# Kernel optimization log

Measured on AMD Instinct MI355X. Metric: run time of the kernel, lower is better.

The kernel has to match this reference:

```python
import jax, jax.numpy as jnp
import numpy as np

NEG_INF = -jnp.inf


def conv2d(x, w, b, stride, pad):
    # x: [B,C,H,W], w: [O,I,kh,kw]
    y = jax.lax.conv_general_dilated(
        x, w, window_strides=(stride, stride),
        padding=[(pad, pad), (pad, pad)],
        dimension_numbers=('NCHW', 'OIHW', 'NCHW'))
    return y + b[None, :, None, None]


def maxpool3s2(x):
    return jax.lax.reduce_window(x, -jnp.inf, jax.lax.max,
                                 (1, 1, 3, 3), (1, 1, 2, 2), 'VALID')


def setup_inputs() -> dict:
    key = jax.random.key(0)
    ks = jax.random.split(key, 20)
    s = 0.02
    B, C, H, W = 64, 3, 224, 224
    D, HID, OUT, E = 9216, 288, 1000, 8   # feature_dim, hidden_dim, output_dim, n_experts
    GH = 72                               # gate hidden = hidden_dim // 4
    inp = {
        'x':   jax.random.normal(ks[0], (B, C, H, W), jnp.float32),
        'c1w': s * jax.random.normal(ks[1], (64, 3, 11, 11), jnp.float32),
        'c1b': jnp.zeros((64,), jnp.float32),
        'c2w': s * jax.random.normal(ks[2], (192, 64, 5, 5), jnp.float32),
        'c2b': jnp.zeros((192,), jnp.float32),
        'c3w': s * jax.random.normal(ks[3], (384, 192, 3, 3), jnp.float32),
        'c3b': jnp.zeros((384,), jnp.float32),
        'c4w': s * jax.random.normal(ks[4], (256, 384, 3, 3), jnp.float32),
        'c4b': jnp.zeros((256,), jnp.float32),
        'c5w': s * jax.random.normal(ks[5], (256, 256, 3, 3), jnp.float32),
        'c5b': jnp.zeros((256,), jnp.float32),
        'gw1': s * jax.random.normal(ks[6], (D, GH), jnp.float32),
        'gb1': jnp.zeros((GH,), jnp.float32),
        'gw2': s * jax.random.normal(ks[7], (GH, E), jnp.float32),
        'gb2': jnp.zeros((E,), jnp.float32),
        'ew1': s * jax.random.normal(ks[8], (E, D, HID), jnp.float32),
        'eb1': jnp.zeros((E, HID), jnp.float32),
        'ew2': s * jax.random.normal(ks[9], (E, HID, HID // 2), jnp.float32),
        'eb2': jnp.zeros((E, HID // 2), jnp.float32),
        'ew3': s * jax.random.normal(ks[10], (E, HID // 2, OUT), jnp.float32),
        'eb3': jnp.zeros((E, OUT), jnp.float32),
    }
    return inp


def reference(x, c1w, c1b, c2w, c2b, c3w, c3b, c4w, c4b, c5w, c5b,
              gw1, gb1, gw2, gb2, ew1, eb1, ew2, eb2, ew3, eb3):
    # ---- AlexNet-style feature extractor (224 branch) ----
    h = jax.nn.relu(conv2d(x, c1w, c1b, 4, 2))   # [B,64,55,55]
    h = maxpool3s2(h)                             # [B,64,27,27]
    h = jax.nn.relu(conv2d(h, c2w, c2b, 1, 2))   # [B,192,27,27]
    h = maxpool3s2(h)                             # [B,192,13,13]
    h = jax.nn.relu(conv2d(h, c3w, c3b, 1, 1))   # [B,384,13,13]
    h = jax.nn.relu(conv2d(h, c4w, c4b, 1, 1))   # [B,256,13,13]
    h = jax.nn.relu(conv2d(h, c5w, c5b, 1, 1))   # [B,256,13,13]
    h = maxpool3s2(h)                             # [B,256,6,6]
    # AdaptiveAvgPool2d((6,6)) on a 6x6 input is the identity.
    feat = h.reshape(h.shape[0], -1)              # [B,9216]

    # ---- Gate: top-2 routing (eval mode: no noise, no dropout) ----
    g = jax.nn.relu(feat @ gw1 + gb1)             # [B,72]
    logits = g @ gw2 + gb2                        # [B,8]
    topv, topi = jax.lax.top_k(logits, 2)         # [B,2]
    topw = jax.nn.softmax(topv, axis=-1)          # softmax over top-2 only
    B = logits.shape[0]
    gates = jnp.zeros_like(logits).at[jnp.arange(B)[:, None], topi].set(topw)  # [B,8]

    # ---- Dense per-expert 3-layer MLP over full batch (as in source) ----
    h1 = jax.nn.relu(jnp.einsum('bd,edh->ebh', feat, ew1) + eb1[:, None, :])   # [E,B,288]
    h2 = jax.nn.relu(jnp.einsum('ebh,ehk->ebk', h1, ew2) + eb2[:, None, :])    # [E,B,144]
    eo = jnp.einsum('ebk,eko->ebo', h2, ew3) + eb3[:, None, :]                 # [E,B,1000]
    # Weighted combine; gates are zero for non-top-2 experts, matching the
    # masked accumulation loop in the torch forward.
    out = jnp.einsum('ebo,be->bo', eo, gates)     # [B,1000]
    return out
```

## Files before the change

kernel.cpp:

```cpp
#include <hip/hip_runtime.h>
#include <math.h>

#define TPB 256

typedef short s16x8 __attribute__((ext_vector_type(8)));
typedef short s16x4 __attribute__((ext_vector_type(4)));
typedef float f32x4 __attribute__((ext_vector_type(4)));

__device__ inline void bsplit(float x, short& h, short& l){
  union { float f; unsigned u; } a, hf, rf;
  a.f = x;
  unsigned hu = (a.u + 0x7FFFu + ((a.u >> 16) & 1u)) >> 16;
  h = (short)hu;
  hf.u = hu << 16;
  rf.f = x - hf.f;
  l = (short)((rf.u + 0x7FFFu + ((rf.u >> 16) & 1u)) >> 16);
}
__device__ inline float b2f(short s){
  union { unsigned u; float f; } x;
  x.u = ((unsigned)(unsigned short)s) << 16;
  return x.f;
}

__global__ __launch_bounds__(TPB) void wsplit_k(
    const float* __restrict__ w, short* __restrict__ wh, short* __restrict__ wl,
    int C, int O, int ntap, int total)
{
  int idx = blockIdx.x*TPB + threadIdx.x;
  if (idx >= total) return;
  int c   = idx % C;
  int t2  = idx / C;
  int oc  = t2 % O;
  int tap = t2 / O;
  float x = w[((size_t)oc*C + c)*ntap + tap];
  short h, l; bsplit(x, h, l);
  int tile = oc >> 4, ln = oc & 15;
  int S    = ntap*(C >> 5);
  int sl   = tap*(C >> 5) + (c >> 5);
  int lg   = (c >> 3) & 3, j = c & 7;
  size_t dst = (((size_t)tile*S + sl)*64 + lg*16 + ln)*8 + j;
  wh[dst] = h; wl[dst] = l;
}

__global__ __launch_bounds__(TPB) void wsplit1_k(
    const float* __restrict__ w, short* __restrict__ wh, short* __restrict__ wl)
{
  int idx = blockIdx.x*TPB + threadIdx.x;
  if (idx >= 64*576) return;
  int k  = idx % 576;
  int oc = idx / 576;
  int g  = k >> 4, kw = k & 15;
  int c  = g / 12, kh = g % 12;
  float x = 0.f;
  if (kh < 11 && kw < 11)
    x = w[((size_t)oc*3 + c)*121 + kh*11 + kw];
  short h, l; bsplit(x, h, l);
  int m = oc >> 4, ln = oc & 15;
  int s = k >> 5, r = k & 31;
  int lg = r >> 3, j = r & 7;
  size_t dst = (((size_t)m*18 + s)*64 + lg*16 + ln)*8 + j;
  wh[dst] = h; wl[dst] = l;
}

__global__ __launch_bounds__(TPB) void wtrans_k(
    const float* __restrict__ w, float* __restrict__ wT, int K, int O)
{
  int idx = blockIdx.x*TPB + threadIdx.x;
  if (idx >= K*O) return;
  int oc = idx % O;
  int k  = idx / O;
  wT[idx] = w[(size_t)oc*K + k];
}

#define C1W 240
#define CV1_PL 33
__global__ __launch_bounds__(256, 2) void conv1m_k(
    const float* __restrict__ in, const short* __restrict__ whi,
    const short* __restrict__ wlo, const float* __restrict__ bias,
    short* __restrict__ yh, short* __restrict__ yl)
{
  __shared__ __align__(16) short lds[2][CV1_PL*C1W + 84];
  const int tid = threadIdx.x;
  const int oh = blockIdx.x % 55;
  const int b  = blockIdx.x / 55;
  const int nt = tid >> 6;
  const int ln = tid & 15;
  const int lg = (tid & 63) >> 4;
  const int lane = tid & 63;
  const int ow = nt*16 + ln;

  const float* ip = in + (size_t)b*3*224*224;
  for (int i = tid; i < CV1_PL*59; i += 256){
    int plane = i / 59;
    int p     = i % 59;
    int c = plane / 11, kh = plane % 11;
    int ih = oh*4 - 2 + kh;
    int col0 = p*4;
    const float* rowp = (ih >= 0 && ih < 224) ? ip + (size_t)c*50176 + (size_t)ih*224 : nullptr;
    short h[4], l[4];
    #pragma unroll
    for (int j=0;j<4;++j){
      int iw = col0 + j - 2;
      float v = (rowp && iw >= 0 && iw < 224) ? rowp[iw] : 0.f;
      bsplit(v, h[j], l[j]);
    }
    s16x4 hv = {h[0],h[1],h[2],h[3]}, lv = {l[0],l[1],l[2],l[3]};
    *reinterpret_cast<s16x4*>(&lds[0][plane*C1W + col0]) = hv;
    *reinterpret_cast<s16x4*>(&lds[1][plane*C1W + col0]) = lv;
  }
  __syncthreads();

  f32x4 acc[4];
  #pragma unroll
  for (int m=0;m<4;++m){
    const float4 bv = *reinterpret_cast<const float4*>(bias + m*16 + lg*4);
    acc[m] = (f32x4){bv.x, bv.y, bv.z, bv.w};
  }

  s16x8 ah[4], al[4], ahn[4], aln[4];
  #pragma unroll
  for (int m=0;m<4;++m){
    size_t ao = (((size_t)m*18 + 0)*64 + lane)*8;
    ah[m] = *reinterpret_cast<const s16x8*>(whi + ao);
    al[m] = *reinterpret_cast<const s16x8*>(wlo + ao);
  }

  #pragma unroll 1
  for (int s=0; s<18; ++s){
    if (s < 17){
      #pragma unroll
      for (int m=0;m<4;++m){
        size_t ao = (((size_t)m*18 + s + 1)*64 + lane)*8;
        ahn[m] = *reinterpret_cast<const s16x8*>(whi + ao);
        aln[m] = *reinterpret_cast<const s16x8*>(wlo + ao);
      }
    }
    int g  = 2*s + (lg >> 1);
    int c  = g / 12, kh = g % 12;
    int plane = c*11 + (kh < 11 ? kh : 10);
    int base  = plane*C1W + ow*4 + (lg & 1)*8;
    s16x4 h0 = *reinterpret_cast<const s16x4*>(&lds[0][base]);
    s16x4 h1 = *reinterpret_cast<const s16x4*>(&lds[0][base+4]);
    s16x4 l0 = *reinterpret_cast<const s16x4*>(&lds[1][base]);
    s16x4 l1 = *reinterpret_cast<const s16x4*>(&lds[1][base+4]);
    s16x8 bh = __builtin_shufflevector(h0, h1, 0,1,2,3,4,5,6,7);
    s16x8 bl = __builtin_shufflevector(l0, l1, 0,1,2,3,4,5,6,7);
    #pragma unroll
    for (int m=0;m<4;++m){
      acc[m] = __builtin_amdgcn_mfma_f32_16x16x32_bf16(al[m], bh, acc[m], 0,0,0);
      acc[m] = __builtin_amdgcn_mfma_f32_16x16x32_bf16(ah[m], bl, acc[m], 0,0,0);
      acc[m] = __builtin_amdgcn_mfma_f32_16x16x32_bf16(ah[m], bh, acc[m], 0,0,0);
    }
    #pragma unroll
    for (int m=0;m<4;++m){ ah[m] = ahn[m]; al[m] = aln[m]; }
  }

  if (ow < 55){
    size_t base = ((size_t)b*3025 + (size_t)oh*55 + ow)*64;
    #pragma unroll
    for (int m=0;m<4;++m){
      short h[4], l[4];
      #pragma unroll
      for (int r=0;r<4;++r) bsplit(fmaxf(acc[m][r], 0.f), h[r], l[r]);
      s16x4 hv = {h[0],h[1],h[2],h[3]}, lv = {l[0],l[1],l[2],l[3]};
      *reinterpret_cast<s16x4*>(yh + base + m*16 + lg*4) = hv;
      *reinterpret_cast<s16x4*>(yl + base + m*16 + lg*4) = lv;
    }
  }
}

__global__ __launch_bounds__(TPB) void pool1_k(
    const short* __restrict__ xh, const short* __restrict__ xl,
    short* __restrict__ yh, short* __restrict__ yl)
{
  int i = blockIdx.x*TPB + threadIdx.x;
  if (i >= 64*729*64) return;
  int c = i & 63;
  int t = i >> 6;
  int sp = t % 729;
  int b = t / 729;
  int r = sp/27, cc = sp%27;
  const short* ph = xh + (size_t)b*3025*64 + c;
  const short* pl = xl + (size_t)b*3025*64 + c;
  float m = -INFINITY;
  #pragma unroll
  for (int di=0;di<3;++di)
    #pragma unroll
    for (int dj=0;dj<3;++dj){
      size_t s = (size_t)((2*r+di)*55 + 2*cc+dj)*64;
      m = fmaxf(m, b2f(ph[s]) + b2f(pl[s]));
    }
  short h, l; bsplit(m, h, l);
  yh[i] = h; yl[i] = l;
}

__global__ __launch_bounds__(256, 3) void conv2m_k(
    const short* __restrict__ xh, const short* __restrict__ xl,
    const short* __restrict__ whi, const short* __restrict__ wlo,
    const float* __restrict__ bias, short* __restrict__ yh, short* __restrict__ yl)
{
  __shared__ __align__(16) short lds[2][217*40];
  const int tid = threadIdx.x;
  const int rg  = blockIdx.x;
  const int b   = blockIdx.y;
  const int wid = tid >> 6;
  const int ln  = tid & 15;
  const int lg  = (tid & 63) >> 4;
  const int lane = tid & 63;
  const int oc0 = wid*48;
  const int r0  = rg*3;

  int sb[6], nn[6];
  #pragma unroll
  for (int t=0;t<6;++t){
    int n = t*16 + ln;
    nn[t] = n;
    int ohl = n / 27, ow = n % 27;
    sb[t] = (n < 81) ? (ohl*31 + ow) : 0;
  }

  f32x4 acc[3][6];
  #pragma unroll
  for (int m=0;m<3;++m){
    const float4 bv = *reinterpret_cast<const float4*>(bias + oc0 + m*16 + lg*4);
    #pragma unroll
    for (int t=0;t<6;++t) acc[m][t] = (f32x4){bv.x, bv.y, bv.z, bv.w};
  }

  #pragma unroll 1
  for (int c0=0; c0<64; c0+=32){
    __syncthreads();
    for (int i = tid; i < 217*4; i += 256){
      int sp = i >> 2, v = i & 3;
      int pr = sp/31, pc = sp%31;
      int ih = r0 - 2 + pr, iw = pc - 2;
      s16x8 hv = {0,0,0,0,0,0,0,0}, lv = {0,0,0,0,0,0,0,0};
      if (ih >= 0 && ih < 27 && iw >= 0 && iw < 27){
        size_t o = ((size_t)b*729 + ih*27 + iw)*64 + c0 + v*8;
        hv = *reinterpret_cast<const s16x8*>(xh + o);
        lv = *reinterpret_cast<const s16x8*>(xl + o);
      }
      *reinterpret_cast<s16x8*>(&lds[0][sp*40 + v*8]) = hv;
      *reinterpret_cast<s16x8*>(&lds[1][sp*40 + v*8]) = lv;
    }
    __syncthreads();

    const size_t tstr = 50*512;
    const size_t abase = ((size_t)(wid*3)*50 + (c0 >> 5))*512 + (size_t)lane*8;
    s16x8 ah0 = *reinterpret_cast<const s16x8*>(whi + abase);
    s16x8 ah1 = *reinterpret_cast<const s16x8*>(whi + abase + tstr);
    s16x8 ah2 = *reinterpret_cast<const s16x8*>(whi + abase + 2*tstr);
    s16x8 al0 = *reinterpret_cast<const s16x8*>(wlo + abase);
    s16x8 al1 = *reinterpret_cast<const s16x8*>(wlo + abase + tstr);
    s16x8 al2 = *reinterpret_cast<const s16x8*>(wlo + abase + 2*tstr);

    #pragma unroll 1
    for (int tap=0; tap<25; ++tap){
      s16x8 nh0=ah0, nh1=ah1, nh2=ah2, nl0=al0, nl1=al1, nl2=al2;
      if (tap < 24){
        size_t ao = abase + (size_t)(tap+1)*2*512;
        nh0 = *reinterpret_cast<const s16x8*>(whi + ao);
        nh1 = *reinterpret_cast<const s16x8*>(whi + ao + tstr);
        nh2 = *reinterpret_cast<const s16x8*>(whi + ao + 2*tstr);
        nl0 = *reinterpret_cast<const s16x8*>(wlo + ao);
        nl1 = *reinterpret_cast<const s16x8*>(wlo + ao + tstr);
        nl2 = *reinterpret_cast<const s16x8*>(wlo + ao + 2*tstr);
      }
      const int toff = (tap/5)*31 + (tap%5);
      #pragma unroll
      for (int t=0;t<6;++t){
        int off = (sb[t] + toff)*40 + lg*8;
        s16x8 bh = *reinterpret_cast<const s16x8*>(&lds[0][off]);
        s16x8 bl = *reinterpret_cast<const s16x8*>(&lds[1][off]);
        acc[0][t] = __builtin_amdgcn_mfma_f32_16x16x32_bf16(al0, bh, acc[0][t], 0,0,0);
        acc[0][t] = __builtin_amdgcn_mfma_f32_16x16x32_bf16(ah0, bl, acc[0][t], 0,0,0);
        acc[0][t] = __builtin_amdgcn_mfma_f32_16x16x32_bf16(ah0, bh, acc[0][t], 0,0,0);
        acc[1][t] = __builtin_amdgcn_mfma_f32_16x16x32_bf16(al1, bh, acc[1][t], 0,0,0);
        acc[1][t] = __builtin_amdgcn_mfma_f32_16x16x32_bf16(ah1, bl, acc[1][t], 0,0,0);
        acc[1][t] = __builtin_amdgcn_mfma_f32_16x16x32_bf16(ah1, bh, acc[1][t], 0,0,0);
        acc[2][t] = __builtin_amdgcn_mfma_f32_16x16x32_bf16(al2, bh, acc[2][t], 0,0,0);
        acc[2][t] = __builtin_amdgcn_mfma_f32_16x16x32_bf16(ah2, bl, acc[2][t], 0,0,0);
        acc[2][t] = __builtin_amdgcn_mfma_f32_16x16x32_bf16(ah2, bh, acc[2][t], 0,0,0);
      }
      ah0=nh0; ah1=nh1; ah2=nh2; al0=nl0; al1=nl1; al2=nl2;
    }
  }

  #pragma unroll
  for (int m=0;m<3;++m)
    #pragma unroll
    for (int t=0;t<6;++t){
      if (nn[t] < 81){
        int gsp = r0*27 + nn[t];
        size_t base = ((size_t)b*729 + gsp)*192 + oc0 + m*16 + lg*4;
        short h[4], l[4];
        #pragma unroll
        for (int r=0;r<4;++r) bsplit(fmaxf(acc[m][t][r], 0.f), h[r], l[r]);
        s16x4 hv = {h[0],h[1],h[2],h[3]}, lv = {l[0],l[1],l[2],l[3]};
        *reinterpret_cast<s16x4*>(yh + base) = hv;
        *reinterpret_cast<s16x4*>(yl + base) = lv;
      }
    }
}

__global__ __launch_bounds__(TPB) void pool2_k(
    const short* __restrict__ xh, const short* __restrict__ xl,
    short* __restrict__ yh, short* __restrict__ yl)
{
  int i = blockIdx.x*TPB + threadIdx.x;
  if (i >= 64*169*192) return;
  int c = i % 192;
  int t = i / 192;
  int sp = t % 169;
  int b = t / 169;
  int r = sp/13, cc = sp%13;
  const short* ph = xh + (size_t)b*729*192 + c;
  const short* pl = xl + (size_t)b*729*192 + c;
  float m = -INFINITY;
  #pragma unroll
  for (int di=0;di<3;++di)
    #pragma unroll
    for (int dj=0;dj<3;++dj){
      size_t s = (size_t)((2*r+di)*27 + 2*cc+dj)*192;
      m = fmaxf(m, b2f(ph[s]) + b2f(pl[s]));
    }
  short h, l; bsplit(m, h, l);
  yh[i] = h; yl[i] = l;
}

template<int C,int O>
__global__ __launch_bounds__(256, 3) void conv3m_k(
    const short* __restrict__ xh, const short* __restrict__ xl,
    const short* __restrict__ whi, const short* __restrict__ wlo,
    const float* __restrict__ bias, short* __restrict__ yh, short* __restrict__ yl)
{
  __shared__ __align__(16) short lds[2][225*40];
  const int tid = threadIdx.x;
  const int b   = blockIdx.y;
  const int wid = tid >> 6;
  const int ln  = tid & 15;
  const int lg  = (tid & 63) >> 4;
  const int lane = tid & 63;
  const int tileIdx = blockIdx.x*2 + (wid & 1);
  const int oc0 = tileIdx*16;
  const int ng  = wid >> 1;
  const int tbase  = ng ? 6 : 0;
  const int ntiles = ng ? 5 : 6;
  const int S3 = 9*(C/32);

  int sb[6], nn[6];
  #pragma unroll
  for (int t=0;t<6;++t){
    int n = (tbase + t)*16 + ln;
    nn[t] = n;
    int oh = n / 13, ow = n % 13;
    sb[t] = (n < 169) ? (oh*15 + ow) : 0;
  }

  f32x4 acc[6];
  const float4 bv = *reinterpret_cast<const float4*>(bias + oc0 + lg*4);
  #pragma unroll
  for (int t=0;t<6;++t) acc[t] = (f32x4){bv.x, bv.y, bv.z, bv.w};

  #pragma unroll 1
  for (int c0=0; c0<C; c0+=32){
    __syncthreads();
    for (int i = tid; i < 225*4; i += 256){
      int sp = i >> 2, v = i & 3;
      int r = sp/15, cc = sp%15;
      s16x8 hv = {0,0,0,0,0,0,0,0}, lv = {0,0,0,0,0,0,0,0};
      if (r >= 1 && r <= 13 && cc >= 1 && cc <= 13){
        size_t o = ((size_t)b*169 + (r-1)*13 + (cc-1))*C + c0 + v*8;
        hv = *reinterpret_cast<const s16x8*>(xh + o);
        lv = *reinterpret_cast<const s16x8*>(xl + o);
      }
      *reinterpret_cast<s16x8*>(&lds[0][sp*40 + v*8]) = hv;
      *reinterpret_cast<s16x8*>(&lds[1][sp*40 + v*8]) = lv;
    }
    __syncthreads();

    const size_t tb = (size_t)tileIdx*S3 + (c0 >> 5);
    s16x8 ah = *reinterpret_cast<const s16x8*>(whi + (tb*64 + lane)*8);
    s16x8 al = *reinterpret_cast<const s16x8*>(wlo + (tb*64 + lane)*8);
    #pragma unroll 1
    for (int tap=0; tap<9; ++tap){
      s16x8 ahn = ah, aln = al;
      if (tap < 8){
        size_t ao = ((tb + (size_t)(tap+1)*(C/32))*64 + lane)*8;
        ahn = *reinterpret_cast<const s16x8*>(whi + ao);
        aln = *reinterpret_cast<const s16x8*>(wlo + ao);
      }
      const int toff = (tap/3)*15 + (tap%3);
      #pragma unroll
      for (int t=0;t<6;++t){
        if (t < ntiles){
          int off = (sb[t] + toff)*40 + lg*8;
          s16x8 bh = *reinterpret_cast<const s16x8*>(&lds[0][off]);
          s16x8 bl = *reinterpret_cast<const s16x8*>(&lds[1][off]);
          acc[t] = __builtin_amdgcn_mfma_f32_16x16x32_bf16(al, bh, acc[t], 0,0,0);
          acc[t] = __builtin_amdgcn_mfma_f32_16x16x32_bf16(ah, bl, acc[t], 0,0,0);
          acc[t] = __builtin_amdgcn_mfma_f32_16x16x32_bf16(ah, bh, acc[t], 0,0,0);
        }
      }
      ah = ahn; al = aln;
    }
  }

  #pragma unroll
  for (int t=0;t<6;++t){
    if (t < ntiles && nn[t] < 169){
      size_t base = ((size_t)b*169 + nn[t])*O + oc0 + lg*4;
      short h[4], l[4];
      #pragma unroll
      for (int r=0;r<4;++r) bsplit(fmaxf(acc[t][r], 0.f), h[r], l[r]);
      s16x4 hv = {h[0],h[1],h[2],h[3]}, lv = {l[0],l[1],l[2],l[3]};
      *reinterpret_cast<s16x4*>(yh + base) = hv;
      *reinterpret_cast<s16x4*>(yl + base) = lv;
    }
  }
}

__global__ __launch_bounds__(TPB) void pool3_k(
    const short* __restrict__ xh, const short* __restrict__ xl,
    float* __restrict__ feat)
{
  int i = blockIdx.x*TPB + threadIdx.x;
  if (i >= 64*9216) return;
  int d = i % 9216;
  int b = i / 9216;
  int c = d / 36;
  int sp = d % 36;
  int r = sp/6, cc = sp%6;
  const short* ph = xh + (size_t)b*169*256 + c;
  const short* pl = xl + (size_t)b*169*256 + c;
  float m = -INFINITY;
  #pragma unroll
  for (int di=0;di<3;++di)
    #pragma unroll
    for (int dj=0;dj<3;++dj){
      size_t s = (size_t)((2*r+di)*13 + 2*cc+dj)*256;
      m = fmaxf(m, b2f(ph[s]) + b2f(pl[s]));
    }
  feat[i] = m;
}

__global__ __launch_bounds__(256) void gate1_k(
    const float* __restrict__ feat, const float* __restrict__ gw1T,
    const float* __restrict__ gb1, float* __restrict__ g)
{
  const int b    = blockIdx.x;
  const int h    = blockIdx.y*4 + (threadIdx.x >> 6);
  const int lane = threadIdx.x & 63;
  const float* f = feat + (size_t)b*9216;
  const float* w = gw1T + (size_t)h*9216;
  float s = 0.f;
  #pragma unroll
  for (int it=0; it<36; ++it){
    int d = it*256 + lane*4;
    float4 fv = *reinterpret_cast<const float4*>(f + d);
    float4 wv = *reinterpret_cast<const float4*>(w + d);
    s = fmaf(fv.x, wv.x, s);
    s = fmaf(fv.y, wv.y, s);
    s = fmaf(fv.z, wv.z, s);
    s = fmaf(fv.w, wv.w, s);
  }
  #pragma unroll
  for (int off=32; off; off>>=1) s += __shfl_down(s, off, 64);
  if (lane == 0) g[(size_t)b*72 + h] = fmaxf(s + gb1[h], 0.f);
}

__global__ __launch_bounds__(128) void gate2_k(
    const float* __restrict__ g, const float* __restrict__ gw2,
    const float* __restrict__ gb2, float* __restrict__ gates)
{
  const int b = blockIdx.x;
  const int tid = threadIdx.x;
  __shared__ float gs[72];
  __shared__ float logits[8];
  if (tid < 72) gs[tid] = g[(size_t)b*72 + tid];
  __syncthreads();
  if (tid < 8) {
    float acc = gb2[tid];
    for (int j=0;j<72;++j)
      acc = fmaf(gs[j], gw2[(size_t)j*8 + tid], acc);
    logits[tid] = acc;
  }
  __syncthreads();
  if (tid == 0) {
    int i1 = 0; float v1 = logits[0];
    for (int e=1;e<8;++e) if (logits[e] > v1) { v1 = logits[e]; i1 = e; }
    int i2 = -1; float v2 = -INFINITY;
    for (int e=0;e<8;++e) { if (e==i1) continue; if (logits[e] > v2) { v2 = logits[e]; i2 = e; } }
    float z  = expf(v2 - v1);
    float w1 = 1.f / (1.f + z);
    float w2 = z   / (1.f + z);
    float* gr = gates + (size_t)b*8;
    for (int e=0;e<8;++e) gr[e] = 0.f;
    gr[i1] = w1;
    gr[i2] = w2;
  }
}

__global__ __launch_bounds__(256, 2) void eh1_part_k(
    const float* __restrict__ feat, const float* __restrict__ ew1,
    float* __restrict__ part)
{
  const int e  = blockIdx.x;
  const int ks = blockIdx.y;
  const int nb = blockIdx.z;
  const int h0 = nb*144;
  __shared__ __align__(16) float fs[64*33];
  __shared__ __align__(16) float wsh[32*144];
  const int tid = threadIdx.x;
  const int tx = tid & 15;
  const int ty = tid >> 4;
  float acc[4][9];
  #pragma unroll
  for (int i=0;i<4;++i)
    #pragma unroll
    for (int j=0;j<9;++j) acc[i][j]=0.f;
  const float* wbase = ew1 + (size_t)e*9216*288 + h0;
  for (int d0 = ks*192; d0 < ks*192+192; d0 += 32){
    __syncthreads();
    for (int l = tid; l < 512; l += 256){
      int r = l >> 3, c = l & 7;
      float4 v = *reinterpret_cast<const float4*>(feat + (size_t)r*9216 + d0 + c*4);
      float* dst = &fs[r*33 + c*4];
      dst[0]=v.x; dst[1]=v.y; dst[2]=v.z; dst[3]=v.w;
    }
    for (int l = tid; l < 1152; l += 256){
      int r = l / 36, c = l % 36;
      *reinterpret_cast<float4*>(&wsh[r*144 + c*4]) =
        *reinterpret_cast<const float4*>(wbase + (size_t)(d0 + r)*288 + c*4);
    }
    __syncthreads();
    #pragma unroll
    for (int k=0;k<32;++k){
      float fv[4], wv[9];
      #pragma unroll
      for (int i=0;i<4;++i) fv[i] = fs[(ty*4+i)*33 + k];
      #pragma unroll
      for (int j=0;j<9;++j) wv[j] = wsh[k*144 + tx*9 + j];
      #pragma unroll
      for (int i=0;i<4;++i)
        #pragma unroll
        for (int j=0;j<9;++j)
          acc[i][j] = fmaf(fv[i], wv[j], acc[i][j]);
    }
  }
  float* pp = part + (size_t)(ks*8 + e)*64*288;
  #pragma unroll
  for (int i=0;i<4;++i)
    #pragma unroll
    for (int j=0;j<9;++j)
      pp[(ty*4+i)*288 + h0 + tx*9 + j] = acc[i][j];
}

__global__ __launch_bounds__(TPB) void eh1_reduce_k(
    const float* __restrict__ part, const float* __restrict__ eb1,
    float* __restrict__ h1)
{
  int idx = blockIdx.x*TPB + threadIdx.x;
  if (idx >= 8*64*288) return;
  int h = idx % 288;
  int e = idx / (64*288);
  float a = eb1[(size_t)e*288 + h];
  #pragma unroll
  for (int s=0;s<48;++s)
    a += part[(size_t)s*147456 + idx];
  h1[idx] = fmaxf(a, 0.f);
}

__global__ __launch_bounds__(TPB) void expert_h2_k(
    const float* __restrict__ h1, const float* __restrict__ ew2,
    const float* __restrict__ eb2, const float* __restrict__ gates,
    float* __restrict__ h2)
{
  int idx = blockIdx.x*TPB + threadIdx.x;
  if (idx >= 8*64*144) return;
  int k = idx % 144;
  int t = idx / 144;
  int b = t % 64;
  int e = t / 64;
  if (gates[(size_t)b*8 + e] == 0.f) return;
  float acc = eb2[(size_t)e*144 + k];
  const float* h = h1 + ((size_t)e*64 + b)*288;
  const float* w = ew2 + (size_t)e*288*144 + k;
  for (int d=0; d<288; ++d)
    acc = fmaf(h[d], w[(size_t)d*144], acc);
  h2[idx] = fmaxf(acc, 0.f);
}

__global__ __launch_bounds__(TPB) void expert_out_k(
    const float* __restrict__ h2, const float* __restrict__ ew3,
    const float* __restrict__ eb3, const float* __restrict__ gates,
    float* __restrict__ out)
{
  int idx = blockIdx.x*TPB + threadIdx.x;
  if (idx >= 64*1000) return;
  int o = idx % 1000;
  int b = idx / 1000;
  float acc = 0.f;
  const float* gr = gates + (size_t)b*8;
  for (int e=0;e<8;++e){
    float ge = gr[e];
    if (ge == 0.f) continue;
    float a = eb3[(size_t)e*1000 + o];
    const float* h = h2 + ((size_t)e*64 + b)*144;
    const float* w = ew3 + (size_t)e*144*1000 + o;
    for (int k=0;k<144;++k)
      a = fmaf(h[k], w[(size_t)k*1000], a);
    acc = fmaf(ge, a, acc);
  }
  out[idx] = acc;
}

static inline int nblk(long long n){ return (int)((n + TPB - 1) / TPB); }

extern "C" void kernel_launch(void* const* d_in, const int* in_sizes, int n_in,
                              void* d_out, int out_size, void* d_ws, size_t ws_size,
                              hipStream_t stream)
{
  const float* x   = (const float*)d_in[0];
  const float* c1w = (const float*)d_in[1];  const float* c1b = (const float*)d_in[2];
  const float* c2w = (const float*)d_in[3];  const float* c2b = (const float*)d_in[4];
  const float* c3w = (const float*)d_in[5];  const float* c3b = (const float*)d_in[6];
  const float* c4w = (const float*)d_in[7];  const float* c4b = (const float*)d_in[8];
  const float* c5w = (const float*)d_in[9];  const float* c5b = (const float*)d_in[10];
  const float* gw1 = (const float*)d_in[11]; const float* gb1 = (const float*)d_in[12];
  const float* gw2 = (const float*)d_in[13]; const float* gb2 = (const float*)d_in[14];
  const float* ew1 = (const float*)d_in[15]; const float* eb1 = (const float*)d_in[16];
  const float* ew2 = (const float*)d_in[17]; const float* eb2 = (const float*)d_in[18];
  const float* ew3 = (const float*)d_in[19]; const float* eb3 = (const float*)d_in[20];
  float* out = (float*)d_out;

  float* W = (float*)d_ws;
  short* X1H = (short*)W;
  short* X1L = X1H + 12390400;
  short* X3H = (short*)W;
  short* X3L = X3H + 8957952;
  short* X5H = (short*)W;
  short* X5L = X5H + 4153344;
  short* X7H = (short*)W;
  short* X7L = X7H + 2768896;
  float* feat  = W + 5000000;
  float* part  = W + 6000000;
  short* WH2 = (short*)(W +  9000000);
  short* WL2 = WH2 + 307200;
  short* WH3 = (short*)(W +  9320000);
  short* WL3 = WH3 + 663552;
  short* WH4 = (short*)(W + 10000000);
  short* WL4 = WH4 + 884736;
  short* WH5 = (short*)(W + 10900000);
  short* WL5 = WH5 + 589824;
  float* GT1 = W + 11500000;
  short* X2H = (short*)(W + 12390400);
  short* X2L = X2H + 2985984;
  short* X4H = (short*)(W + 12390400);
  short* X4L = X4H + 2076672;
  short* X6H = (short*)(W + 12390400);
  short* X6L = X6H + 2768896;
  float* gates = W + 14000000;
  float* h1    = gates + 512;
  float* h2    = h1 + 147456;
  float* gbuf  = h2 + 73728;
  short* WH1 = (short*)(W + 15400000);
  short* WL1 = WH1 + 36864;
  (void)ws_size; (void)in_sizes; (void)n_in; (void)out_size;

  wsplit1_k<<<nblk(64LL*576), TPB, 0, stream>>>(c1w, WH1, WL1);
  conv1m_k<<<55*64, 256, 0, stream>>>(x, WH1, WL1, c1b, X1H, X1L);
  pool1_k<<<nblk(64LL*729*64), TPB, 0, stream>>>(X1H, X1L, X2H, X2L);
  wsplit_k<<<nblk(25LL*192*64),  TPB, 0, stream>>>(c2w, WH2, WL2,  64, 192, 25, 25*192*64);
  wsplit_k<<<nblk(9LL*384*192),  TPB, 0, stream>>>(c3w, WH3, WL3, 192, 384,  9, 9*384*192);
  wsplit_k<<<nblk(9LL*256*384),  TPB, 0, stream>>>(c4w, WH4, WL4, 384, 256,  9, 9*256*384);
  wsplit_k<<<nblk(9LL*256*256),  TPB, 0, stream>>>(c5w, WH5, WL5, 256, 256,  9, 9*256*256);
  wtrans_k<<<nblk(72LL*9216),    TPB, 0, stream>>>(gw1, GT1, 72, 9216);

  conv2m_k<<<dim3(9,64), 256, 0, stream>>>(X2H, X2L, WH2, WL2, c2b, X3H, X3L);
  pool2_k<<<nblk(64LL*169*192), TPB, 0, stream>>>(X3H, X3L, X4H, X4L);
  conv3m_k<192,384><<<dim3(12,64), 256, 0, stream>>>(X4H, X4L, WH3, WL3, c3b, X5H, X5L);
  conv3m_k<384,256><<<dim3(8,64),  256, 0, stream>>>(X5H, X5L, WH4, WL4, c4b, X6H, X6L);
  conv3m_k<256,256><<<dim3(8,64),  256, 0, stream>>>(X6H, X6L, WH5, WL5, c5b, X7H, X7L);
  pool3_k<<<nblk(64LL*9216), TPB, 0, stream>>>(X7H, X7L, feat);

  gate1_k<<<dim3(64,18), 256, 0, stream>>>(feat, GT1, gb1, gbuf);
  gate2_k<<<64, 128, 0, stream>>>(gbuf, gw2, gb2, gates);

  eh1_part_k<<<dim3(8,48,2), 256, 0, stream>>>(feat, ew1, part);
  eh1_reduce_k<<<nblk(8LL*64*288), TPB, 0, stream>>>(part, eb1, h1);
  expert_h2_k<<<nblk(8LL*64*144), TPB, 0, stream>>>(h1, ew2, eb2, gates, h2);
  expert_out_k<<<nblk(64LL*1000), TPB, 0, stream>>>(h2, ew3, eb3, gates, out);
}
```

Baseline: 585.1 us.

## Move expert layer-1 GEMM to split-bf16 MFMA and raise conv occupancy bounds

Replaces the FP32 SIMT expert first-layer GEMM (64x9216 by 8x9216x288) with an MFMA kernel that uses three-term bf16 hi/lo splitting. Features are pre-split into an MFMA-friendly layout by a new kernel, and weights are split on the fly into LDS. The split-K factor drops from 48 to 16, and the reduce kernel is adapted to the new partial layout. Separately, launch_bounds min-blocks on the conv kernels is raised to 4, which may force register spills.

```diff
diff --git a/kernel.cpp b/kernel.cpp
--- a/kernel.cpp
+++ b/kernel.cpp
@@ -74,7 +74,7 @@
 
 #define C1W 240
 #define CV1_PL 33
-__global__ __launch_bounds__(256, 2) void conv1m_k(
+__global__ __launch_bounds__(256, 4) void conv1m_k(
     const float* __restrict__ in, const short* __restrict__ whi,
     const short* __restrict__ wlo, const float* __restrict__ bias,
     short* __restrict__ yh, short* __restrict__ yl)
@@ -194,7 +194,7 @@
   yh[i] = h; yl[i] = l;
 }
 
-__global__ __launch_bounds__(256, 3) void conv2m_k(
+__global__ __launch_bounds__(256, 4) void conv2m_k(
     const short* __restrict__ xh, const short* __restrict__ xl,
     const short* __restrict__ whi, const short* __restrict__ wlo,
     const float* __restrict__ bias, short* __restrict__ yh, short* __restrict__ yl)
@@ -329,7 +329,7 @@
 }
 
 template<int C,int O>
-__global__ __launch_bounds__(256, 3) void conv3m_k(
+__global__ __launch_bounds__(256, 4) void conv3m_k(
     const short* __restrict__ xh, const short* __restrict__ xl,
     const short* __restrict__ whi, const short* __restrict__ wlo,
     const float* __restrict__ bias, short* __restrict__ yh, short* __restrict__ yl)
@@ -444,6 +444,21 @@
   feat[i] = m;
 }
 
+__global__ __launch_bounds__(TPB) void featsplit_k(
+    const float* __restrict__ feat, short* __restrict__ fbh, short* __restrict__ fbl)
+{
+  int idx = blockIdx.x*TPB + threadIdx.x;
+  if (idx >= 589824) return;
+  int j = idx & 7;
+  int lane = (idx >> 3) & 63;
+  int nt = (idx >> 9) & 3;
+  int s = idx >> 11;
+  int b = nt*16 + (lane & 15);
+  int d = s*32 + (lane >> 4)*8 + j;
+  short h, l; bsplit(feat[(size_t)b*9216 + d], h, l);
+  fbh[idx] = h; fbl[idx] = l;
+}
+
 __global__ __launch_bounds__(256) void gate1_k(
     const float* __restrict__ feat, const float* __restrict__ gw1T,
     const float* __restrict__ gb1, float* __restrict__ g)
@@ -501,59 +516,70 @@
   }
 }
 
-__global__ __launch_bounds__(256, 2) void eh1_part_k(
-    const float* __restrict__ feat, const float* __restrict__ ew1,
-    float* __restrict__ part)
-{
-  const int e  = blockIdx.x;
-  const int ks = blockIdx.y;
-  const int nb = blockIdx.z;
-  const int h0 = nb*144;
-  __shared__ __align__(16) float fs[64*33];
-  __shared__ __align__(16) float wsh[32*144];
+__global__ __launch_bounds__(256, 4) void eh1m_k(
+    const float* __restrict__ ew1, const short* __restrict__ fbh,
+    const short* __restrict__ fbl, float* __restrict__ part)
+{
+  __shared__ __align__(16) short wh_l[32*88];
+  __shared__ __align__(16) short wl_l[32*88];
+  const int m2 = blockIdx.x;
+  const int e  = blockIdx.y;
+  const int ks = blockIdx.z;
   const int tid = threadIdx.x;
-  const int tx = tid & 15;
-  const int ty = tid >> 4;
-  float acc[4][9];
-  #pragma unroll
-  for (int i=0;i<4;++i)
-    #pragma unroll
-    for (int j=0;j<9;++j) acc[i][j]=0.f;
-  const float* wbase = ew1 + (size_t)e*9216*288 + h0;
-  for (int d0 = ks*192; d0 < ks*192+192; d0 += 32){
+  const int nt = tid >> 6;
+  const int ln = tid & 15;
+  const int lg = (tid & 63) >> 4;
+  const int lane = tid & 63;
+
+  f32x4 acc[2] = {(f32x4){0.f,0.f,0.f,0.f},(f32x4){0.f,0.f,0.f,0.f}};
+
+  const float* wsrc = ew1 + (size_t)e*9216*288 + (size_t)m2*32;
+  const int d0 = ks*576;
+
+  #pragma unroll 1
+  for (int st=0; st<9; ++st){
     __syncthreads();
-    for (int l = tid; l < 512; l += 256){
-      int r = l >> 3, c = l & 7;
-      float4 v = *reinterpret_cast<const float4*>(feat + (size_t)r*9216 + d0 + c*4);
-      float* dst = &fs[r*33 + c*4];
-      dst[0]=v.x; dst[1]=v.y; dst[2]=v.z; dst[3]=v.w;
-    }
-    for (int l = tid; l < 1152; l += 256){
-      int r = l / 36, c = l % 36;
-      *reinterpret_cast<float4*>(&wsh[r*144 + c*4]) =
-        *reinterpret_cast<const float4*>(wbase + (size_t)(d0 + r)*288 + c*4);
+    {
+      int drow = tid >> 2;
+      int h0 = (tid & 3)*8;
+      const float* src = wsrc + (size_t)(d0 + st*64 + drow)*288 + h0;
+      float4 v0 = *reinterpret_cast<const float4*>(src);
+      float4 v1 = *reinterpret_cast<const float4*>(src+4);
+      float vv[8] = {v0.x,v0.y,v0.z,v0.w,v1.x,v1.y,v1.z,v1.w};
+      #pragma unroll
+      for (int k=0;k<8;++k){
+        short h, l; bsplit(vv[k], h, l);
+        wh_l[(h0+k)*88 + drow] = h;
+        wl_l[(h0+k)*88 + drow] = l;
+      }
     }
     __syncthreads();
-    #pragma unroll
-    for (int k=0;k<32;++k){
-      float fv[4], wv[9];
+    int sg = (d0 + st*64) >> 5;
+    #pragma unroll
+    for (int sl=0; sl<2; ++sl){
+      size_t bo = ((size_t)(sg+sl)*4 + nt)*512 + (size_t)lane*8;
+      s16x8 bh = *reinterpret_cast<const s16x8*>(fbh + bo);
+      s16x8 bl = *reinterpret_cast<const s16x8*>(fbl + bo);
       #pragma unroll
-      for (int i=0;i<4;++i) fv[i] = fs[(ty*4+i)*33 + k];
-      #pragma unroll
-      for (int j=0;j<9;++j) wv[j] = wsh[k*144 + tx*9 + j];
-      #pragma unroll
-      for (int i=0;i<4;++i)
-        #pragma unroll
-        for (int j=0;j<9;++j)
-          acc[i][j] = fmaf(fv[i], wv[j], acc[i][j]);
-    }
-  }
-  float* pp = part + (size_t)(ks*8 + e)*64*288;
-  #pragma unroll
-  for (int i=0;i<4;++i)
-    #pragma unroll
-    for (int j=0;j<9;++j)
-      pp[(ty*4+i)*288 + h0 + tx*9 + j] = acc[i][j];
+      for (int m=0;m<2;++m){
+        int ao = (m*16 + ln)*88 + sl*32 + lg*8;
+        s16x8 ah = *reinterpret_cast<const s16x8*>(&wh_l[ao]);
+        s16x8 al = *reinterpret_cast<const s16x8*>(&wl_l[ao]);
+        acc[m] = __builtin_amdgcn_mfma_f32_16x16x32_bf16(al, bh, acc[m], 0,0,0);
+        acc[m] = __builtin_amdgcn_mfma_f32_16x16x32_bf16(ah, bl, acc[m], 0,0,0);
+        acc[m] = __builtin_amdgcn_mfma_f32_16x16x32_bf16(ah, bh, acc[m], 0,0,0);
+      }
+    }
+  }
+  #pragma unroll
+  for (int m=0;m<2;++m){
+    int h = m2*32 + m*16 + lg*4;
+    int b = nt*16 + ln;
+    float* pp = part + ((size_t)(ks*8+e)*288 + h)*64 + b;
+    #pragma unroll
+    for (int r=0;r<4;++r)
+      pp[(size_t)r*64] = acc[m][r];
+  }
 }
 
 __global__ __launch_bounds__(TPB) void eh1_reduce_k(
@@ -561,14 +587,15 @@
     float* __restrict__ h1)
 {
   int idx = blockIdx.x*TPB + threadIdx.x;
-  if (idx >= 8*64*288) return;
-  int h = idx % 288;
+  if (idx >= 8*288*64) return;
+  int b = idx & 63;
+  int h = (idx >> 6) % 288;
   int e = idx / (64*288);
   float a = eb1[(size_t)e*288 + h];
   #pragma unroll
-  for (int s=0;s<48;++s)
-    a += part[(size_t)s*147456 + idx];
-  h1[idx] = fmaxf(a, 0.f);
+  for (int s=0;s<16;++s)
+    a += part[((size_t)(s*8+e)*288 + h)*64 + b];
+  h1[((size_t)e*64 + b)*288 + h] = fmaxf(a, 0.f);
 }
 
 __global__ __launch_bounds__(TPB) void expert_h2_k(
@@ -644,7 +671,9 @@
   short* X7H = (short*)W;
   short* X7L = X7H + 2768896;
   float* feat  = W + 5000000;
-  float* part  = W + 6000000;
+  short* FBH   = (short*)(W + 5600000);
+  short* FBL   = (short*)(W + 5900000);
+  float* part  = W + 6300000;
   short* WH2 = (short*)(W +  9000000);
   short* WL2 = WH2 + 307200;
   short* WH3 = (short*)(W +  9320000);
@@ -687,8 +716,9 @@
   gate1_k<<<dim3(64,18), 256, 0, stream>>>(feat, GT1, gb1, gbuf);
   gate2_k<<<64, 128, 0, stream>>>(gbuf, gw2, gb2, gates);
 
-  eh1_part_k<<<dim3(8,48,2), 256, 0, stream>>>(feat, ew1, part);
-  eh1_reduce_k<<<nblk(8LL*64*288), TPB, 0, stream>>>(part, eb1, h1);
+  featsplit_k<<<nblk(589824LL), TPB, 0, stream>>>(feat, FBH, FBL);
+  eh1m_k<<<dim3(9,8,16), 256, 0, stream>>>(ew1, FBH, FBL, part);
+  eh1_reduce_k<<<nblk(8LL*288*64), TPB, 0, stream>>>(part, eb1, h1);
   expert_h2_k<<<nblk(8LL*64*144), TPB, 0, stream>>>(h1, ew2, eb2, gates, h2);
   expert_out_k<<<nblk(64LL*1000), TPB, 0, stream>>>(h2, ew3, eb3, gates, out);
 }
```

New measurement: 576.3 us. Within noise of the previous version (-1.5%).
